# Kernel tuning notes

Hardware: AMD Instinct MI355X
Metric: run time of the kernel (lower is better)

The kernel has to match this reference:

```python
import jax, jax.numpy as jnp
import numpy as np

N, E = 50000, 500000          # nodes per type, edges per message type
F_IN, H, L = 128, 128, 8      # input feat, hidden_size, num_labels
EPS, SLOPE = 1e-5, 0.01       # BatchNorm eps, LeakyReLU slope


def setup_inputs() -> dict:
    key = jax.random.key(0)
    ks = jax.random.split(key, 16)
    s = 0.05
    d = {}
    d["x_n0"] = jax.random.normal(ks[0], (N, F_IN), jnp.float32)
    d["x_n1"] = jax.random.normal(ks[1], (N, F_IN), jnp.float32)
    # stacked per-message-type SAGE params (3 message types), two layers
    d["Wn1"] = jax.random.normal(ks[2], (3, F_IN, H), jnp.float32) * s
    d["Ws1"] = jax.random.normal(ks[3], (3, F_IN, H), jnp.float32) * s
    d["Wu1"] = jax.random.normal(ks[4], (3, 2 * H, H), jnp.float32) * s
    d["Wn2"] = jax.random.normal(ks[5], (3, H, H), jnp.float32) * s
    d["Ws2"] = jax.random.normal(ks[6], (3, H, H), jnp.float32) * s
    d["Wu2"] = jax.random.normal(ks[7], (3, 2 * H, H), jnp.float32) * s
    for nm in ("bn1", "bs1", "bu1", "bn2", "bs2", "bu2"):
        d[nm] = jnp.zeros((3, H), jnp.float32)
    # per-node-type BatchNorm affine params (2 node types), two layers
    d["gamma1"] = jnp.ones((2, H), jnp.float32)
    d["beta1"] = jnp.zeros((2, H), jnp.float32)
    d["gamma2"] = jnp.ones((2, H), jnp.float32)
    d["beta2"] = jnp.zeros((2, H), jnp.float32)
    # per-node-type post-MP linear
    d["Wp"] = jax.random.normal(ks[8], (2, H, L), jnp.float32) * s
    d["bp"] = jnp.zeros((2, L), jnp.float32)
    # edge_index per message type: [2, E] with row0=src, row1=dst
    d["ei0"] = jax.random.randint(ks[9], (2, E), 0, N, jnp.int32)   # n0 -> n1
    d["ei1"] = jax.random.randint(ks[10], (2, E), 0, N, jnp.int32)  # n1 -> n0
    d["ei2"] = jax.random.randint(ks[11], (2, E), 0, N, jnp.int32)  # n0 -> n0
    return d


def _segment_mean(x, idx, n):
    s = jax.ops.segment_sum(x, idx, num_segments=n)
    c = jax.ops.segment_sum(jnp.ones((idx.shape[0], 1), x.dtype), idx, num_segments=n)
    return s / jnp.maximum(c, 1.0)


def _sage(x_src, x_dst, ei, Wn, bn, Ws, bs, Wu, bu):
    # gather source feats per edge, scatter-mean to dst, then linear branches
    agg = _segment_mean(x_src[ei[0]], ei[1], x_dst.shape[0])  # [N_dst, F]
    h = jnp.concatenate([agg @ Wn + bn, x_dst @ Ws + bs], axis=-1)
    return h @ Wu + bu


def _bn(x, g, b):
    m = x.mean(0)
    v = ((x - m) ** 2).mean(0)  # biased variance, as torch BN training mode
    return (x - m) * jax.lax.rsqrt(v + EPS) * g + b


def _lrelu(x):
    return jnp.where(x >= 0, x, SLOPE * x)


def _layer(x0, x1, ei0, ei1, ei2, Wn, bn, Ws, bs, Wu, bu, gamma, beta):
    m0 = _sage(x0, x1, ei0, Wn[0], bn[0], Ws[0], bs[0], Wu[0], bu[0])  # dst n1
    m1 = _sage(x1, x0, ei1, Wn[1], bn[1], Ws[1], bs[1], Wu[1], bu[1])  # dst n0
    m2 = _sage(x0, x0, ei2, Wn[2], bn[2], Ws[2], bs[2], Wu[2], bu[2])  # dst n0
    h0 = 0.5 * (m1 + m2)   # mean over the 2 message types targeting n0
    h1 = m0                # single message type for n1
    h0 = _lrelu(_bn(h0, gamma[0], beta[0]))
    h1 = _lrelu(_bn(h1, gamma[1], beta[1]))
    return h0, h1


def reference(x_n0, x_n1, Wn1, bn1, Ws1, bs1, Wu1, bu1,
              Wn2, bn2, Ws2, bs2, Wu2, bu2,
              gamma1, beta1, gamma2, beta2, Wp, bp, ei0, ei1, ei2):
    h0, h1 = _layer(x_n0, x_n1, ei0, ei1, ei2, Wn1, bn1, Ws1, bs1, Wu1, bu1, gamma1, beta1)
    h0, h1 = _layer(h0, h1, ei0, ei1, ei2, Wn2, bn2, Ws2, bs2, Wu2, bu2, gamma2, beta2)
    out0 = h0 @ Wp[0] + bp[0]
    out1 = h1 @ Wp[1] + bp[1]
    return jnp.stack([out0, out1])  # [2, N, L]
```

## Files before the change

kernel.cpp:

```cpp
#include <hip/hip_runtime.h>

#define LBL 8
#define NBMAX 128
#define BSH 9
#define BCAP 8192

typedef __attribute__((ext_vector_type(8))) short short8;
typedef __attribute__((ext_vector_type(4))) float f32x4;

__device__ __forceinline__ uint f2bf(float x) {
    uint u = __float_as_uint(x);
    return (u + 0x7fffu + ((u >> 16) & 1u)) >> 16;
}
__device__ __forceinline__ float bflo(uint v) { return __uint_as_float(v << 16); }
__device__ __forceinline__ float bfhi(uint v) { return __uint_as_float(v & 0xffff0000u); }

__global__ void f2b2(const float4* __restrict__ x0, const float4* __restrict__ x1,
                     uint2* __restrict__ o0, uint2* __restrict__ o1, int n4) {
    int y = blockIdx.y;
    const float4* in = y ? x1 : x0;
    uint2* out = y ? o1 : o0;
    int i = blockIdx.x * blockDim.x + threadIdx.x;
    int stride = gridDim.x * blockDim.x;
    for (; i < n4; i += stride) {
        float4 v = in[i];
        uint2 o;
        o.x = f2bf(v.x) | (f2bf(v.y) << 16);
        o.y = f2bf(v.z) | (f2bf(v.w) << 16);
        out[i] = o;
    }
}


__global__ void bhist3(const int* __restrict__ e0, const int* __restrict__ e1,
                       const int* __restrict__ e2, int E, int NB, int* __restrict__ bcnt) {
    int m = blockIdx.y;
    const int* dst = (m == 0 ? e0 : (m == 1 ? e1 : e2)) + E;
    __shared__ int h[NBMAX];
    int tid = threadIdx.x;
    if (tid < NB) h[tid] = 0;
    __syncthreads();
    int i = blockIdx.x * blockDim.x + tid, st = gridDim.x * blockDim.x;
    for (; i < E; i += st) atomicAdd(&h[dst[i] >> BSH], 1);
    __syncthreads();
    if (tid < NB && h[tid]) atomicAdd(&bcnt[m * NB + tid], h[tid]);
}

__global__ void bscan(const int* __restrict__ bcnt, int* __restrict__ bso,
                      int* __restrict__ gcur, int NB) {
    int m = threadIdx.x;
    if (m >= 3) return;
    int acc = 0;
    for (int b = 0; b < NB; ++b) {
        bso[m * (NB + 1) + b] = acc;
        gcur[m * NB + b] = acc;
        acc += bcnt[m * NB + b];
    }
    bso[m * (NB + 1) + NB] = acc;
}

#define BIN_CH 16
__global__ __launch_bounds__(256) void bin3(const int* __restrict__ e0, const int* __restrict__ e1,
                                            const int* __restrict__ e2, int E, int NB,
                                            int* __restrict__ gcur, uint* __restrict__ pairs) {
    int m = blockIdx.y;
    const int* eb = (m == 0 ? e0 : (m == 1 ? e1 : e2));
    const int* src = eb;
    const int* dst = eb + E;
    uint* pp = pairs + (size_t)m * E;
    int* gc = gcur + m * NB;
    __shared__ int h[NBMAX], base[NBMAX], pos[NBMAX];
    int tid = threadIdx.x;
    if (tid < NB) { h[tid] = 0; pos[tid] = 0; }
    __syncthreads();
    int i0 = blockIdx.x * (256 * BIN_CH);
    uint pk[BIN_CH];
    int bk[BIN_CH];
    #pragma unroll
    for (int u = 0; u < BIN_CH; ++u) {
        int i = i0 + u * 256 + tid;
        bk[u] = -1;
        if (i < E) {
            int s = src[i], d = dst[i];
            bk[u] = d >> BSH;
            pk[u] = (uint)s | ((uint)(d & ((1 << BSH) - 1)) << 16);
            atomicAdd(&h[bk[u]], 1);
        }
    }
    __syncthreads();
    if (tid < NB && h[tid]) base[tid] = atomicAdd(&gc[tid], h[tid]);
    __syncthreads();
    #pragma unroll
    for (int u = 0; u < BIN_CH; ++u) {
        if (bk[u] >= 0) {
            int p = base[bk[u]] + atomicAdd(&pos[bk[u]], 1);
            pp[p] = pk[u];
        }
    }
}

__global__ __launch_bounds__(256) void csr3(const uint* __restrict__ pairs, const int* __restrict__ bso,
                                            int E, int N, int NB,
                                            int* __restrict__ offs, int* __restrict__ srcs) {
    int m = blockIdx.y, b = blockIdx.x;
    const uint* pp = pairs + (size_t)m * E;
    int gstart = bso[m * (NB + 1) + b];
    int gend = bso[m * (NB + 1) + b + 1];
    int cnt = gend - gstart;
    if (cnt > BCAP) cnt = BCAP;
    int d0 = b << BSH;
    int dcnt = N - d0;
    if (dcnt > (1 << BSH)) dcnt = 1 << BSH;

    __shared__ int hist[1 << BSH], po[1 << BSH], off0[1 << BSH];
    __shared__ int lsort[BCAP];
    __shared__ int wsum[4];
    int tid = threadIdx.x;
    hist[tid] = 0;
    hist[tid + 256] = 0;
    __syncthreads();
    for (int i = tid; i < cnt; i += 256) atomicAdd(&hist[pp[gstart + i] >> 16], 1);
    __syncthreads();
    int a = hist[2 * tid], b2 = hist[2 * tid + 1];
    int s = a + b2;
    int lane = tid & 63, w = tid >> 6;
    #pragma unroll
    for (int o = 1; o < 64; o <<= 1) {
        int v = __shfl_up(s, o, 64);
        if (lane >= o) s += v;
    }
    if (lane == 63) wsum[w] = s;
    __syncthreads();
    int wp = 0;
    #pragma unroll
    for (int q = 0; q < 4; ++q)
        if (q < w) wp += wsum[q];
    int excl = wp + s - a - b2;
    off0[2 * tid] = excl; off0[2 * tid + 1] = excl + a;
    po[2 * tid] = excl;   po[2 * tid + 1] = excl + a;
    __syncthreads();
    for (int j = tid; j < dcnt; j += 256) offs[(size_t)m * (N + 1) + d0 + j] = gstart + off0[j];
    if (b == NB - 1 && tid == 0) offs[(size_t)m * (N + 1) + N] = bso[m * (NB + 1) + NB];
    for (int i = tid; i < cnt; i += 256) {
        uint e = pp[gstart + i];
        int p = atomicAdd(&po[e >> 16], 1);
        if (p < BCAP) lsort[p] = (int)(e & 0xffffu);
    }
    __syncthreads();
    for (int i = tid; i < cnt; i += 256) srcs[(size_t)m * E + gstart + i] = lsort[i];
}

__global__ void agg3(const ushort* __restrict__ s0, const ushort* __restrict__ s1,
                     const ushort* __restrict__ s2,
                     uint* __restrict__ o0, uint* __restrict__ o1, uint* __restrict__ o2,
                     const int* __restrict__ offs, const int* __restrict__ srcs,
                     int n, int E) {
    int m = blockIdx.y;
    const uint4* x = (const uint4*)(m == 0 ? s0 : (m == 1 ? s1 : s2));
    uint4* o = (uint4*)(m == 0 ? o0 : (m == 1 ? o1 : o2));
    const int* off = offs + (size_t)m * (n + 1);
    const int* sl = srcs + (size_t)m * E;

    int tid = threadIdx.x;
    int l16 = tid & 15;
    int row = blockIdx.x * 16 + (tid >> 4);
    if (row >= n) return;
    int s = off[row], e = off[row + 1];
    float a0 = 0, a1 = 0, a2 = 0, a3 = 0, a4 = 0, a5 = 0, a6 = 0, a7 = 0;
    int i = s;
    for (; i + 3 < e; i += 4) {
        int j0 = sl[i], j1 = sl[i + 1], j2 = sl[i + 2], j3 = sl[i + 3];
        uint4 v0 = x[(size_t)j0 * 16 + l16];
        uint4 v1 = x[(size_t)j1 * 16 + l16];
        uint4 v2 = x[(size_t)j2 * 16 + l16];
        uint4 v3 = x[(size_t)j3 * 16 + l16];
        a0 += (bflo(v0.x) + bflo(v1.x)) + (bflo(v2.x) + bflo(v3.x));
        a1 += (bfhi(v0.x) + bfhi(v1.x)) + (bfhi(v2.x) + bfhi(v3.x));
        a2 += (bflo(v0.y) + bflo(v1.y)) + (bflo(v2.y) + bflo(v3.y));
        a3 += (bfhi(v0.y) + bfhi(v1.y)) + (bfhi(v2.y) + bfhi(v3.y));
        a4 += (bflo(v0.z) + bflo(v1.z)) + (bflo(v2.z) + bflo(v3.z));
        a5 += (bfhi(v0.z) + bfhi(v1.z)) + (bfhi(v2.z) + bfhi(v3.z));
        a6 += (bflo(v0.w) + bflo(v1.w)) + (bflo(v2.w) + bflo(v3.w));
        a7 += (bfhi(v0.w) + bfhi(v1.w)) + (bfhi(v2.w) + bfhi(v3.w));
    }
    for (; i < e; ++i) {
        uint4 v = x[(size_t)sl[i] * 16 + l16];
        a0 += bflo(v.x); a1 += bfhi(v.x);
        a2 += bflo(v.y); a3 += bfhi(v.y);
        a4 += bflo(v.z); a5 += bfhi(v.z);
        a6 += bflo(v.w); a7 += bfhi(v.w);
    }
    int d = e - s;
    float inv = 1.f / (float)(d > 0 ? d : 1);
    uint4 r;
    r.x = f2bf(a0 * inv) | (f2bf(a1 * inv) << 16);
    r.y = f2bf(a2 * inv) | (f2bf(a3 * inv) << 16);
    r.z = f2bf(a4 * inv) | (f2bf(a5 * inv) << 16);
    r.w = f2bf(a6 * inv) | (f2bf(a7 * inv) << 16);
    o[(size_t)row * 16 + l16] = r;
}

__global__ void fuseW(const float* __restrict__ Wn1, const float* __restrict__ Ws1,
                      const float* __restrict__ Wu1,
                      const float* __restrict__ Wn2, const float* __restrict__ Ws2,
                      const float* __restrict__ Wu2, ushort* __restrict__ FT) {
    int j5 = blockIdx.y;
    int l = j5 / 5, t = j5 - l * 5;
    const float* Wn = l ? Wn2 : Wn1;
    const float* Ws = l ? Ws2 : Ws1;
    const float* Wu = l ? Wu2 : Wu1;
    const float *A0, *B0, *A1 = nullptr, *B1 = nullptr;
    float al;
    switch (t) {
        case 0: A0 = Wn;          B0 = Wu;          al = 1.0f; break;
        case 1: A0 = Wn + 16384;  B0 = Wu + 32768;  al = 0.5f; break;
        case 2: A0 = Wn + 32768;  B0 = Wu + 65536;  al = 0.5f; break;
        case 3: A0 = Ws;          B0 = Wu + 16384;  al = 1.0f; break;
        default:
            A0 = Ws + 16384; B0 = Wu + 49152;
            A1 = Ws + 32768; B1 = Wu + 81920;
            al = 0.5f; break;
    }
    int i = blockIdx.x, j = threadIdx.x;
    float s0 = 0, s1 = 0, s2 = 0, s3 = 0;
    #pragma unroll 4
    for (int k = 0; k < 128; k += 4) {
        s0 += A0[i * 128 + k]     * B0[k * 128 + j];
        s1 += A0[i * 128 + k + 1] * B0[(k + 1) * 128 + j];
        s2 += A0[i * 128 + k + 2] * B0[(k + 2) * 128 + j];
        s3 += A0[i * 128 + k + 3] * B0[(k + 3) * 128 + j];
    }
    if (A1) {
        #pragma unroll 4
        for (int k = 0; k < 128; k += 4) {
            s0 += A1[i * 128 + k]     * B1[k * 128 + j];
            s1 += A1[i * 128 + k + 1] * B1[(k + 1) * 128 + j];
            s2 += A1[i * 128 + k + 2] * B1[(k + 2) * 128 + j];
            s3 += A1[i * 128 + k + 3] * B1[(k + 3) * 128 + j];
        }
    }
    float r = al * ((s0 + s1) + (s2 + s3));
    FT[(size_t)j5 * 16384 + j * 128 + i] = (ushort)f2bf(r);
}

__global__ void fuseB(const float* __restrict__ bn1, const float* __restrict__ bs1,
                      const float* __restrict__ bu1, const float* __restrict__ Wu1,
                      const float* __restrict__ bn2, const float* __restrict__ bs2,
                      const float* __restrict__ bu2, const float* __restrict__ Wu2,
                      float* __restrict__ FC) {
    int jb = blockIdx.x;
    int l = jb >> 1, which = jb & 1;
    const float* bn = l ? bn2 : bn1;
    const float* bs = l ? bs2 : bs1;
    const float* bu = l ? bu2 : bu1;
    const float* Wu = l ? Wu2 : Wu1;
    int j = threadIdx.x;
    float s = 0.f;
    if (which == 0) {
        s = bu[j];
        for (int k = 0; k < 128; ++k)
            s += bn[k] * Wu[k * 128 + j] + bs[k] * Wu[(128 + k) * 128 + j];
    } else {
        #pragma unroll
        for (int tt = 1; tt <= 2; ++tt) {
            const float* Wt = Wu + tt * 32768;
            float p = bu[tt * 128 + j];
            for (int k = 0; k < 128; ++k)
                p += bn[tt * 128 + k] * Wt[k * 128 + j] + bs[tt * 128 + k] * Wt[(128 + k) * 128 + j];
            s += 0.5f * p;
        }
    }
    FC[jb * 128 + j] = s;
}

__global__ __launch_bounds__(256) void gemm2_mfma(
    const ushort* __restrict__ Aq0, const ushort* __restrict__ Wq0,
    const ushort* __restrict__ Aq1, const ushort* __restrict__ Wq1,
    const ushort* __restrict__ Ap0, const ushort* __restrict__ Wp0,
    const ushort* __restrict__ Ap1, const ushort* __restrict__ Wp1,
    const ushort* __restrict__ Ap2, const ushort* __restrict__ Wp2,
    const float* __restrict__ biasq, const float* __restrict__ biasp,
    ushort* __restrict__ Cq, ushort* __restrict__ Cp, int M,
    float* __restrict__ STW) {
    __shared__ ushort As[64 * 128];
    int y = blockIdx.y;
    const float* bias = y ? biasp : biasq;
    ushort* C = y ? Cp : Cq;
    float* colsum = STW + (size_t)(blockIdx.x & 31) * 512 + (y ? 0 : 256);
    float* colsq = colsum + 128;

    int tid = threadIdx.x;
    int wid = tid >> 6;
    int lane = tid & 63;
    int l15 = lane & 15, lg = lane >> 4;
    int row0 = blockIdx.x * 64;
    int nIn = y ? 3 : 2;

    short8 bw[3][4][2];
    #pragma unroll
    for (int inp = 0; inp < 3; ++inp) {
        const ushort* W = (inp == 0) ? (y ? Wp0 : Wq0)
                        : (inp == 1) ? (y ? Wp1 : Wq1) : Wp2;
        #pragma unroll
        for (int k0 = 0; k0 < 4; ++k0)
            #pragma unroll
            for (int cb = 0; cb < 2; ++cb)
                bw[inp][k0][cb] = *(const short8*)(W + (size_t)(wid * 32 + cb * 16 + l15) * 128 + k0 * 32 + lg * 8);
    }

    f32x4 acc[4][2];
    #pragma unroll
    for (int rb = 0; rb < 4; ++rb)
        #pragma unroll
        for (int cb = 0; cb < 2; ++cb) acc[rb][cb] = (f32x4){0.f, 0.f, 0.f, 0.f};

    int r_ = tid >> 4, ch = tid & 15;
    #pragma unroll
    for (int inp = 0; inp < 3; ++inp) {
        if (inp == 2 && nIn == 2) break;
        const ushort* A = (inp == 0) ? (y ? Ap0 : Aq0)
                        : (inp == 1) ? (y ? Ap1 : Aq1) : Ap2;
        __syncthreads();
        #pragma unroll
        for (int p = 0; p < 4; ++p) {
            int row = p * 16 + r_;
            int gr = row0 + row;
            if (gr > M - 1) gr = M - 1;
            uint4 v = *(const uint4*)(A + (size_t)gr * 128 + ch * 8);
            *(uint4*)&As[row * 128 + ((ch ^ (row & 7)) * 8)] = v;
        }
        __syncthreads();
        #pragma unroll
        for (int k0 = 0; k0 < 4; ++k0) {
            short8 a[4];
            #pragma unroll
            for (int rb = 0; rb < 4; ++rb)
                a[rb] = *(const short8*)&As[(rb * 16 + l15) * 128 + (((k0 * 4 + lg) ^ (l15 & 7)) * 8)];
            #pragma unroll
            for (int rb = 0; rb < 4; ++rb)
                #pragma unroll
                for (int cb = 0; cb < 2; ++cb)
                    acc[rb][cb] = __builtin_amdgcn_mfma_f32_16x16x32_bf16(a[rb], bw[inp][k0][cb], acc[rb][cb], 0, 0, 0);
        }
    }

    float ps[2] = {0.f, 0.f}, pq[2] = {0.f, 0.f};
    int colbase = wid * 32;
    #pragma unroll
    for (int cb = 0; cb < 2; ++cb) {
        int col = colbase + cb * 16 + l15;
        float b = bias[col];
        #pragma unroll
        for (int rb = 0; rb < 4; ++rb) {
            int rbase = row0 + rb * 16 + lg * 4;
            #pragma unroll
            for (int i = 0; i < 4; ++i) {
                int r = rbase + i;
                if (r < M) {
                    float v = acc[rb][cb][i] + b;
                    C[(size_t)r * 128 + col] = (ushort)f2bf(v);
                    ps[cb] += v;
                    pq[cb] += v * v;
                }
            }
        }
    }
    #pragma unroll
    for (int cb = 0; cb < 2; ++cb) {
        ps[cb] += __shfl_xor(ps[cb], 16, 64);
        ps[cb] += __shfl_xor(ps[cb], 32, 64);
        pq[cb] += __shfl_xor(pq[cb], 16, 64);
        pq[cb] += __shfl_xor(pq[cb], 32, 64);
    }
    if (lane < 16) {
        atomicAdd(&colsum[colbase + lane], ps[0]);
        atomicAdd(&colsq[colbase + lane], pq[0]);
        atomicAdd(&colsum[colbase + 16 + lane], ps[1]);
        atomicAdd(&colsq[colbase + 16 + lane], pq[1]);
    }
}

__global__ void bn_fin2(float* __restrict__ STW, float* __restrict__ ST,
                        const float* __restrict__ g0, const float* __restrict__ b0,
                        const float* __restrict__ g1, const float* __restrict__ b1, int N) {
    int tid = threadIdx.x;
    int which = tid >> 7, c = tid & 127;
    float s = 0.f, q = 0.f;
    #pragma unroll 8
    for (int cp = 0; cp < 32; ++cp) {
        s += STW[(size_t)cp * 512 + which * 256 + c];
        q += STW[(size_t)cp * 512 + which * 256 + 128 + c];
    }
    #pragma unroll 8
    for (int cp = 0; cp < 32; ++cp) {
        STW[(size_t)cp * 512 + which * 256 + c] = 0.f;
        STW[(size_t)cp * 512 + which * 256 + 128 + c] = 0.f;
    }
    const float* g = which ? g1 : g0;
    const float* b = which ? b1 : b0;
    float m = s / (float)N;
    float v = q / (float)N - m * m;
    float rs = rsqrtf(v + 1e-5f);
    float sc = g[c] * rs;
    ST[512 + which * 256 + c] = sc;
    ST[640 + which * 256 + c] = b[c] - m * sc;
}

__global__ void bn_apply2(const ushort* __restrict__ Cp, ushort* __restrict__ X0b,
                          const ushort* __restrict__ Cq, ushort* __restrict__ X1b,
                          const float* __restrict__ ST, int n4) {
    int y = blockIdx.y;
    const uint2* in = (const uint2*)(y ? Cq : Cp);
    uint2* out = (uint2*)(y ? X1b : X0b);
    const float* sc = ST + 512 + y * 256;
    const float* sh = sc + 128;
    int i = blockIdx.x * blockDim.x + threadIdx.x;
    int stride = gridDim.x * blockDim.x;
    for (; i < n4; i += stride) {
        uint2 v = in[i];
        int cb = (i * 4) & 127;
        float4 s4 = *(const float4*)&sc[cb];
        float4 h4 = *(const float4*)&sh[cb];
        float y0 = bflo(v.x) * s4.x + h4.x;
        float y1 = bfhi(v.x) * s4.y + h4.y;
        float y2 = bflo(v.y) * s4.z + h4.z;
        float y3 = bfhi(v.y) * s4.w + h4.w;
        y0 = (y0 >= 0.f) ? y0 : 0.01f * y0;
        y1 = (y1 >= 0.f) ? y1 : 0.01f * y1;
        y2 = (y2 >= 0.f) ? y2 : 0.01f * y2;
        y3 = (y3 >= 0.f) ? y3 : 0.01f * y3;
        uint2 o;
        o.x = f2bf(y0) | (f2bf(y1) << 16);
        o.y = f2bf(y2) | (f2bf(y3) << 16);
        out[i] = o;
    }
}

__global__ void projbn2(const ushort* __restrict__ Cp, const ushort* __restrict__ Cq,
                        const float* __restrict__ ST,
                        const float* __restrict__ Wp, const float* __restrict__ bp,
                        float* __restrict__ out, int N) {
    int y = blockIdx.y;
    const uint* h = (const uint*)(y ? Cq : Cp);
    const float* W = Wp + y * 1024;
    const float* b = bp + y * 8;
    float* op = out + (size_t)y * N * 8;
    __shared__ float Wsh[1024];
    __shared__ float scs[128], shs[128];
    __shared__ float bsh[8];
    int tid = threadIdx.x;
    for (int i = tid; i < 1024; i += 256) Wsh[i] = W[i];
    if (tid < 128) {
        scs[tid] = ST[512 + y * 256 + tid];
        shs[tid] = ST[640 + y * 256 + tid];
    }
    if (tid < 8) bsh[tid] = b[tid];
    __syncthreads();
    int idx = blockIdx.x * 256 + tid;
    if (idx >= N * LBL) return;
    int r = idx >> 3, c = idx & 7;
    const uint* hr = h + (size_t)r * 64;
    float s = bsh[c];
    #pragma unroll
    for (int k2 = 0; k2 < 64; ++k2) {
        uint v = hr[k2];
        float xa = bflo(v) * scs[2 * k2] + shs[2 * k2];
        float xb = bfhi(v) * scs[2 * k2 + 1] + shs[2 * k2 + 1];
        xa = (xa >= 0.f) ? xa : 0.01f * xa;
        xb = (xb >= 0.f) ? xb : 0.01f * xb;
        s += xa * Wsh[(2 * k2) * 8 + c] + xb * Wsh[(2 * k2 + 1) * 8 + c];
    }
    op[idx] = s;
}


extern "C" void kernel_launch(void* const* d_in, const int* in_sizes, int n_in,
                              void* d_out, int out_size, void* d_ws, size_t ws_size,
                              hipStream_t stream) {
    const float* x0 = (const float*)d_in[0];
    const float* x1 = (const float*)d_in[1];
    const float* Wn1 = (const float*)d_in[2];
    const float* Ws1 = (const float*)d_in[3];
    const float* Wu1 = (const float*)d_in[4];
    const float* Wn2 = (const float*)d_in[5];
    const float* Ws2 = (const float*)d_in[6];
    const float* Wu2 = (const float*)d_in[7];
    const float* bnn[2] = {(const float*)d_in[8], (const float*)d_in[11]};
    const float* bss[2] = {(const float*)d_in[9], (const float*)d_in[12]};
    const float* buu[2] = {(const float*)d_in[10], (const float*)d_in[13]};
    const float* gam[2] = {(const float*)d_in[14], (const float*)d_in[16]};
    const float* bet[2] = {(const float*)d_in[15], (const float*)d_in[17]};
    const float* Wp = (const float*)d_in[18];
    const float* bp = (const float*)d_in[19];
    const int* ei[3] = {(const int*)d_in[20], (const int*)d_in[21], (const int*)d_in[22]};

    const int N = in_sizes[0] / 128;
    const int E = in_sizes[20] / 2;
    const int NB = (N + (1 << BSH) - 1) >> BSH;
    float* out = (float*)d_out;

    char* wp_ = (char*)d_ws;
    auto carve = [&](size_t bytes) {
        char* r = wp_;
        wp_ += (bytes + 255) & ~(size_t)255;
        return r;
    };
    size_t nodeB = (size_t)N * 128 * sizeof(ushort);
    ushort* Cp = (ushort*)carve(nodeB);
    ushort* Cq = (ushort*)carve(nodeB);
    ushort* Pb = (ushort*)carve(nodeB);
    ushort* Rb = (ushort*)carve(nodeB);
    ushort* Sb = (ushort*)carve(nodeB);
    ushort* X0b = (ushort*)carve(nodeB);
    ushort* X1b = (ushort*)carve(nodeB);
    ushort* x0b = (ushort*)carve(nodeB);
    ushort* x1b = (ushort*)carve(nodeB);
    ushort* FT = (ushort*)carve(10 * 16384 * 2);
    float* FC = (float*)carve(4 * 128 * 4);
    float* ST = (float*)carve(1024 * 4);
    float* STW = (float*)carve(32 * 512 * 4);
    int* offs = (int*)carve((size_t)3 * (N + 1) * 4);
    int* srcs = (int*)carve((size_t)3 * E * 4);
    int* bcnt = (int*)carve((size_t)3 * NB * 4);
    int* bso = (int*)carve((size_t)3 * (NB + 1) * 4);
    int* gcur = (int*)carve((size_t)3 * NB * 4);
    uint* pairs = (uint*)Cp;

    const int ag = (N + 15) / 16;
    const int gg = (N + 63) / 64;
    const int pg = (N * LBL + 255) / 256;
    const int bg = (E + 256 * BIN_CH - 1) / (256 * BIN_CH);

    f2b2<<<dim3(1024, 2), 256, 0, stream>>>((const float4*)x0, (const float4*)x1,
                                            (uint2*)x0b, (uint2*)x1b, N * 32);

    hipMemsetAsync(bcnt, 0, (size_t)3 * NB * 4, stream);
    hipMemsetAsync(STW, 0, 32 * 512 * 4, stream);
    bhist3<<<dim3(512, 3), 256, 0, stream>>>(ei[0], ei[1], ei[2], E, NB, bcnt);
    bscan<<<1, 64, 0, stream>>>(bcnt, bso, gcur, NB);
    bin3<<<dim3(bg, 3), 256, 0, stream>>>(ei[0], ei[1], ei[2], E, NB, gcur, pairs);
    csr3<<<dim3(NB, 3), 256, 0, stream>>>(pairs, bso, E, N, NB, offs, srcs);

    fuseW<<<dim3(128, 10), 128, 0, stream>>>(Wn1, Ws1, Wu1, Wn2, Ws2, Wu2, FT);
    fuseB<<<4, 128, 0, stream>>>(bnn[0], bss[0], buu[0], Wu1, bnn[1], bss[1], buu[1], Wu2, FC);

    const ushort* srcS[2][3] = {{x0b, x1b, x0b}, {X0b, X1b, X0b}};
    const ushort* dstX[2][2] = {{x0b, x1b}, {X0b, X1b}};

    for (int l = 0; l < 2; ++l) {
        const ushort* FA0T = FT + (size_t)(l * 5 + 0) * 16384;
        const ushort* FA1T = FT + (size_t)(l * 5 + 1) * 16384;
        const ushort* FA2T = FT + (size_t)(l * 5 + 2) * 16384;
        const ushort* FB1T = FT + (size_t)(l * 5 + 3) * 16384;
        const ushort* FB0T = FT + (size_t)(l * 5 + 4) * 16384;
        const float* fcH1 = FC + (l * 2 + 0) * 128;
        const float* fcH0 = FC + (l * 2 + 1) * 128;

        agg3<<<dim3(ag, 3), 256, 0, stream>>>(srcS[l][0], srcS[l][1], srcS[l][2],
                                              (uint*)Pb, (uint*)Rb, (uint*)Sb,
                                              offs, srcs, N, E);

        gemm2_mfma<<<dim3(gg, 2), 256, 0, stream>>>(
            Pb, FA0T, dstX[l][1], FB1T,
            Rb, FA1T, Sb, FA2T, dstX[l][0], FB0T,
            fcH1, fcH0, Cq, Cp, N, STW);

        bn_fin2<<<1, 256, 0, stream>>>(STW, ST, gam[l], bet[l], gam[l] + 128, bet[l] + 128, N);
        if (l == 0)
            bn_apply2<<<dim3(1024, 2), 256, 0, stream>>>(Cp, X0b, Cq, X1b, ST, N * 32);
    }

    projbn2<<<dim3(pg, 2), 256, 0, stream>>>(Cp, Cq, ST, Wp, bp, out, N);
}
```

Measured before the change: 311.9 us.

## Use direct global-to-LDS loads in GEMM and unroll aggregation gather by eight

The GEMM kernel now stages A tiles with global_load_lds, so data goes straight from global memory into LDS instead of through registers. The XOR swizzle moves from the LDS destination to the global source address. Weight fragments are now loaded per input inside the loop instead of all up front, which cuts register pressure and may raise occupancy. The aggregation kernel gathers eight neighbours per iteration for more memory-level parallelism, with a two-wide remainder loop; this costs more registers and a changed summation order.

```diff
diff --git a/kernel.cpp b/kernel.cpp
--- a/kernel.cpp
+++ b/kernel.cpp
@@ -14,6 +14,11 @@
 }
 __device__ __forceinline__ float bflo(uint v) { return __uint_as_float(v << 16); }
 __device__ __forceinline__ float bfhi(uint v) { return __uint_as_float(v & 0xffff0000u); }
+
+__device__ __forceinline__ void gload16(const ushort* g, ushort* l) {
+    __builtin_amdgcn_global_load_lds((const __attribute__((address_space(1))) uint*)g,
+                                     (__attribute__((address_space(3))) uint*)l, 16, 0, 0);
+}
 
 __global__ void f2b2(const float4* __restrict__ x0, const float4* __restrict__ x1,
                      uint2* __restrict__ o0, uint2* __restrict__ o1, int n4) {
@@ -168,22 +173,33 @@
     int s = off[row], e = off[row + 1];
     float a0 = 0, a1 = 0, a2 = 0, a3 = 0, a4 = 0, a5 = 0, a6 = 0, a7 = 0;
     int i = s;
-    for (; i + 3 < e; i += 4) {
-        int j0 = sl[i], j1 = sl[i + 1], j2 = sl[i + 2], j3 = sl[i + 3];
-        uint4 v0 = x[(size_t)j0 * 16 + l16];
-        uint4 v1 = x[(size_t)j1 * 16 + l16];
-        uint4 v2 = x[(size_t)j2 * 16 + l16];
-        uint4 v3 = x[(size_t)j3 * 16 + l16];
-        a0 += (bflo(v0.x) + bflo(v1.x)) + (bflo(v2.x) + bflo(v3.x));
-        a1 += (bfhi(v0.x) + bfhi(v1.x)) + (bfhi(v2.x) + bfhi(v3.x));
-        a2 += (bflo(v0.y) + bflo(v1.y)) + (bflo(v2.y) + bflo(v3.y));
-        a3 += (bfhi(v0.y) + bfhi(v1.y)) + (bfhi(v2.y) + bfhi(v3.y));
-        a4 += (bflo(v0.z) + bflo(v1.z)) + (bflo(v2.z) + bflo(v3.z));
-        a5 += (bfhi(v0.z) + bfhi(v1.z)) + (bfhi(v2.z) + bfhi(v3.z));
-        a6 += (bflo(v0.w) + bflo(v1.w)) + (bflo(v2.w) + bflo(v3.w));
-        a7 += (bfhi(v0.w) + bfhi(v1.w)) + (bfhi(v2.w) + bfhi(v3.w));
-    }
-    for (; i < e; ++i) {
+    for (; i + 7 < e; i += 8) {
+        uint4 v0 = x[(size_t)sl[i] * 16 + l16];
+        uint4 v1 = x[(size_t)sl[i + 1] * 16 + l16];
+        uint4 v2 = x[(size_t)sl[i + 2] * 16 + l16];
+        uint4 v3 = x[(size_t)sl[i + 3] * 16 + l16];
+        uint4 v4 = x[(size_t)sl[i + 4] * 16 + l16];
+        uint4 v5 = x[(size_t)sl[i + 5] * 16 + l16];
+        uint4 v6 = x[(size_t)sl[i + 6] * 16 + l16];
+        uint4 v7 = x[(size_t)sl[i + 7] * 16 + l16];
+        a0 += ((bflo(v0.x) + bflo(v1.x)) + (bflo(v2.x) + bflo(v3.x))) + ((bflo(v4.x) + bflo(v5.x)) + (bflo(v6.x) + bflo(v7.x)));
+        a1 += ((bfhi(v0.x) + bfhi(v1.x)) + (bfhi(v2.x) + bfhi(v3.x))) + ((bfhi(v4.x) + bfhi(v5.x)) + (bfhi(v6.x) + bfhi(v7.x)));
+        a2 += ((bflo(v0.y) + bflo(v1.y)) + (bflo(v2.y) + bflo(v3.y))) + ((bflo(v4.y) + bflo(v5.y)) + (bflo(v6.y) + bflo(v7.y)));
+        a3 += ((bfhi(v0.y) + bfhi(v1.y)) + (bfhi(v2.y) + bfhi(v3.y))) + ((bfhi(v4.y) + bfhi(v5.y)) + (bfhi(v6.y) + bfhi(v7.y)));
+        a4 += ((bflo(v0.z) + bflo(v1.z)) + (bflo(v2.z) + bflo(v3.z))) + ((bflo(v4.z) + bflo(v5.z)) + (bflo(v6.z) + bflo(v7.z)));
+        a5 += ((bfhi(v0.z) + bfhi(v1.z)) + (bfhi(v2.z) + bfhi(v3.z))) + ((bfhi(v4.z) + bfhi(v5.z)) + (bfhi(v6.z) + bfhi(v7.z)));
+        a6 += ((bflo(v0.w) + bflo(v1.w)) + (bflo(v2.w) + bflo(v3.w))) + ((bflo(v4.w) + bflo(v5.w)) + (bflo(v6.w) + bflo(v7.w)));
+        a7 += ((bfhi(v0.w) + bfhi(v1.w)) + (bfhi(v2.w) + bfhi(v3.w))) + ((bfhi(v4.w) + bfhi(v5.w)) + (bfhi(v6.w) + bfhi(v7.w)));
+    }
+    for (; i + 1 < e; i += 2) {
+        uint4 v0 = x[(size_t)sl[i] * 16 + l16];
+        uint4 v1 = x[(size_t)sl[i + 1] * 16 + l16];
+        a0 += bflo(v0.x) + bflo(v1.x); a1 += bfhi(v0.x) + bfhi(v1.x);
+        a2 += bflo(v0.y) + bflo(v1.y); a3 += bfhi(v0.y) + bfhi(v1.y);
+        a4 += bflo(v0.z) + bflo(v1.z); a5 += bfhi(v0.z) + bfhi(v1.z);
+        a6 += bflo(v0.w) + bflo(v1.w); a7 += bfhi(v0.w) + bfhi(v1.w);
+    }
+    if (i < e) {
         uint4 v = x[(size_t)sl[i] * 16 + l16];
         a0 += bflo(v.x); a1 += bfhi(v.x);
         a2 += bflo(v.y); a3 += bfhi(v.y);
@@ -296,39 +312,34 @@
     int row0 = blockIdx.x * 64;
     int nIn = y ? 3 : 2;
 
-    short8 bw[3][4][2];
+    f32x4 acc[4][2];
+    #pragma unroll
+    for (int rb = 0; rb < 4; ++rb)
+        #pragma unroll
+        for (int cb = 0; cb < 2; ++cb) acc[rb][cb] = (f32x4){0.f, 0.f, 0.f, 0.f};
+
     #pragma unroll
     for (int inp = 0; inp < 3; ++inp) {
+        if (inp == 2 && nIn == 2) break;
+        const ushort* A = (inp == 0) ? (y ? Ap0 : Aq0)
+                        : (inp == 1) ? (y ? Ap1 : Aq1) : Ap2;
         const ushort* W = (inp == 0) ? (y ? Wp0 : Wq0)
                         : (inp == 1) ? (y ? Wp1 : Wq1) : Wp2;
+        __syncthreads();
+        #pragma unroll
+        for (int p = 0; p < 4; ++p) {
+            int row = wid * 16 + p * 4 + (lane >> 4);
+            int gr = row0 + row;
+            if (gr > M - 1) gr = M - 1;
+            const ushort* src = A + (size_t)gr * 128 + (((lane & 15) ^ (row & 7)) * 8);
+            gload16(src, &As[(wid * 4 + p) * 512]);
+        }
+        short8 bw[4][2];
         #pragma unroll
         for (int k0 = 0; k0 < 4; ++k0)
             #pragma unroll
             for (int cb = 0; cb < 2; ++cb)
-                bw[inp][k0][cb] = *(const short8*)(W + (size_t)(wid * 32 + cb * 16 + l15) * 128 + k0 * 32 + lg * 8);
-    }
-
-    f32x4 acc[4][2];
-    #pragma unroll
-    for (int rb = 0; rb < 4; ++rb)
-        #pragma unroll
-        for (int cb = 0; cb < 2; ++cb) acc[rb][cb] = (f32x4){0.f, 0.f, 0.f, 0.f};
-
-    int r_ = tid >> 4, ch = tid & 15;
-    #pragma unroll
-    for (int inp = 0; inp < 3; ++inp) {
-        if (inp == 2 && nIn == 2) break;
-        const ushort* A = (inp == 0) ? (y ? Ap0 : Aq0)
-                        : (inp == 1) ? (y ? Ap1 : Aq1) : Ap2;
-        __syncthreads();
-        #pragma unroll
-        for (int p = 0; p < 4; ++p) {
-            int row = p * 16 + r_;
-            int gr = row0 + row;
-            if (gr > M - 1) gr = M - 1;
-            uint4 v = *(const uint4*)(A + (size_t)gr * 128 + ch * 8);
-            *(uint4*)&As[row * 128 + ((ch ^ (row & 7)) * 8)] = v;
-        }
+                bw[k0][cb] = *(const short8*)(W + (size_t)(wid * 32 + cb * 16 + l15) * 128 + k0 * 32 + lg * 8);
         __syncthreads();
         #pragma unroll
         for (int k0 = 0; k0 < 4; ++k0) {
@@ -340,7 +351,7 @@
             for (int rb = 0; rb < 4; ++rb)
                 #pragma unroll
                 for (int cb = 0; cb < 2; ++cb)
-                    acc[rb][cb] = __builtin_amdgcn_mfma_f32_16x16x32_bf16(a[rb], bw[inp][k0][cb], acc[rb][cb], 0, 0, 0);
+                    acc[rb][cb] = __builtin_amdgcn_mfma_f32_16x16x32_bf16(a[rb], bw[k0][cb], acc[rb][cb], 0, 0, 0);
         }
     }
 
```

After: 313.2 us. Within noise of the previous version (+0.4%).

## Double-buffer A tiles in gemm2 via direct global-to-LDS loads

Applied to the files above, without the earlier changes.

Stages each input's A tile into LDS with global_load_lds (bypassing registers) and double-buffers it so the next input's tile loads while MFMAs run on the current one. W fragments are now loaded per input instead of all up front, which cuts register pressure. The cost is twice the LDS and a reliance on the swizzled write pattern through the LDS-direct path being correct. Per-input weight loads now sit on the critical path.

```diff
diff --git a/kernel.cpp b/kernel.cpp
--- a/kernel.cpp
+++ b/kernel.cpp
@@ -14,6 +14,11 @@
 }
 __device__ __forceinline__ float bflo(uint v) { return __uint_as_float(v << 16); }
 __device__ __forceinline__ float bfhi(uint v) { return __uint_as_float(v & 0xffff0000u); }
+
+__device__ __forceinline__ void gload16(const ushort* g, ushort* l) {
+    __builtin_amdgcn_global_load_lds((const __attribute__((address_space(1))) uint*)g,
+                                     (__attribute__((address_space(3))) uint*)l, 16, 0, 0);
+}
 
 __global__ void f2b2(const float4* __restrict__ x0, const float4* __restrict__ x1,
                      uint2* __restrict__ o0, uint2* __restrict__ o1, int n4) {
@@ -282,7 +287,7 @@
     const float* __restrict__ biasq, const float* __restrict__ biasp,
     ushort* __restrict__ Cq, ushort* __restrict__ Cp, int M,
     float* __restrict__ STW) {
-    __shared__ ushort As[64 * 128];
+    __shared__ ushort As[2][64 * 128];
     int y = blockIdx.y;
     const float* bias = y ? biasp : biasq;
     ushort* C = y ? Cp : Cq;
@@ -296,52 +301,58 @@
     int row0 = blockIdx.x * 64;
     int nIn = y ? 3 : 2;
 
-    short8 bw[3][4][2];
+    const ushort* Ax[3];
+    const ushort* Wx[3];
+    Ax[0] = y ? Ap0 : Aq0;  Wx[0] = y ? Wp0 : Wq0;
+    Ax[1] = y ? Ap1 : Aq1;  Wx[1] = y ? Wp1 : Wq1;
+    Ax[2] = Ap2;            Wx[2] = Wp2;
+
+    auto stage = [&](const ushort* A, ushort* buf) {
+        #pragma unroll
+        for (int p = 0; p < 4; ++p) {
+            int row = wid * 16 + p * 4 + (lane >> 4);
+            int gr = row0 + row;
+            if (gr > M - 1) gr = M - 1;
+            const ushort* src = A + (size_t)gr * 128 + (((lane & 15) ^ (row & 7)) * 8);
+            gload16(src, buf + (wid * 4 + p) * 512);
+        }
+    };
+
+    f32x4 acc[4][2];
+    #pragma unroll
+    for (int rb = 0; rb < 4; ++rb)
+        #pragma unroll
+        for (int cb = 0; cb < 2; ++cb) acc[rb][cb] = (f32x4){0.f, 0.f, 0.f, 0.f};
+
+    stage(Ax[0], As[0]);
+    __syncthreads();
+    int cur = 0;
+
     #pragma unroll
     for (int inp = 0; inp < 3; ++inp) {
-        const ushort* W = (inp == 0) ? (y ? Wp0 : Wq0)
-                        : (inp == 1) ? (y ? Wp1 : Wq1) : Wp2;
+        if (inp == 2 && nIn == 2) break;
+        const ushort* W = Wx[inp];
+        short8 bw[4][2];
         #pragma unroll
         for (int k0 = 0; k0 < 4; ++k0)
             #pragma unroll
             for (int cb = 0; cb < 2; ++cb)
-                bw[inp][k0][cb] = *(const short8*)(W + (size_t)(wid * 32 + cb * 16 + l15) * 128 + k0 * 32 + lg * 8);
-    }
-
-    f32x4 acc[4][2];
-    #pragma unroll
-    for (int rb = 0; rb < 4; ++rb)
-        #pragma unroll
-        for (int cb = 0; cb < 2; ++cb) acc[rb][cb] = (f32x4){0.f, 0.f, 0.f, 0.f};
-
-    int r_ = tid >> 4, ch = tid & 15;
-    #pragma unroll
-    for (int inp = 0; inp < 3; ++inp) {
-        if (inp == 2 && nIn == 2) break;
-        const ushort* A = (inp == 0) ? (y ? Ap0 : Aq0)
-                        : (inp == 1) ? (y ? Ap1 : Aq1) : Ap2;
-        __syncthreads();
-        #pragma unroll
-        for (int p = 0; p < 4; ++p) {
-            int row = p * 16 + r_;
-            int gr = row0 + row;
-            if (gr > M - 1) gr = M - 1;
-            uint4 v = *(const uint4*)(A + (size_t)gr * 128 + ch * 8);
-            *(uint4*)&As[row * 128 + ((ch ^ (row & 7)) * 8)] = v;
-        }
-        __syncthreads();
+                bw[k0][cb] = *(const short8*)(W + (size_t)(wid * 32 + cb * 16 + l15) * 128 + k0 * 32 + lg * 8);
+        if (inp + 1 < nIn) stage(Ax[inp + 1], As[cur ^ 1]);
         #pragma unroll
         for (int k0 = 0; k0 < 4; ++k0) {
             short8 a[4];
             #pragma unroll
             for (int rb = 0; rb < 4; ++rb)
-                a[rb] = *(const short8*)&As[(rb * 16 + l15) * 128 + (((k0 * 4 + lg) ^ (l15 & 7)) * 8)];
+                a[rb] = *(const short8*)&As[cur][(rb * 16 + l15) * 128 + (((k0 * 4 + lg) ^ (l15 & 7)) * 8)];
             #pragma unroll
             for (int rb = 0; rb < 4; ++rb)
                 #pragma unroll
                 for (int cb = 0; cb < 2; ++cb)
-                    acc[rb][cb] = __builtin_amdgcn_mfma_f32_16x16x32_bf16(a[rb], bw[inp][k0][cb], acc[rb][cb], 0, 0, 0);
-        }
+                    acc[rb][cb] = __builtin_amdgcn_mfma_f32_16x16x32_bf16(a[rb], bw[k0][cb], acc[rb][cb], 0, 0, 0);
+        }
+        __syncthreads();
+        cur ^= 1;
     }
 
     float ps[2] = {0.f, 0.f}, pq[2] = {0.f, 0.f};
```

New measurement: 309.2 us. No clear change (-0.8%).
